# Kernel tuning notes

Measured on AMD Instinct MI355X. Metric: run time of the kernel, lower is better.

Reference implementation:

```python
import jax, jax.numpy as jnp
import numpy as np


def _lstm_step(h, c, x, W, U, b):
    # Keras gate order: i, f, g(candidate), o
    z = x @ W + h @ U + b  # [B, 4H]
    i, f, g, o = jnp.split(z, 4, axis=-1)
    i = jax.nn.sigmoid(i)
    f = jax.nn.sigmoid(f)
    g = jnp.tanh(g)
    o = jax.nn.sigmoid(o)
    c_new = f * c + i * g
    h_new = o * jnp.tanh(c_new)
    return h_new, c_new


def setup_inputs() -> dict:
    key = jax.random.key(0)
    ks = jax.random.split(key, 8)
    B, T, F, H = 2048, 512, 8, 128
    s = lambda k, shape, scale: (jax.random.normal(k, shape, jnp.float32) * scale)
    return {
        "x": jax.random.normal(ks[0], (B, T, F), jnp.float32),
        "W_enc": s(ks[1], (F, 4 * H), 0.1),
        "U_enc": s(ks[2], (H, 4 * H), 0.1),
        "b_enc": jnp.zeros((4 * H,), jnp.float32),
        "W_dec": s(ks[3], (F, 4 * H), 0.1),
        "U_dec": s(ks[4], (H, 4 * H), 0.1),
        "b_dec": jnp.zeros((4 * H,), jnp.float32),
        "W_out": s(ks[5], (H, F), 0.1),
        "b_out": jnp.zeros((F,), jnp.float32),
    }


def reference(x, W_enc, U_enc, b_enc, W_dec, U_dec, b_dec, W_out, b_out):
    B, T, F = x.shape
    H = U_enc.shape[0]
    h0 = jnp.zeros((B, H), x.dtype)
    c0 = jnp.zeros((B, H), x.dtype)

    # Encoder LSTM: only the final (h, c) state is consumed downstream.
    def enc_step(carry, xt):
        h, c = carry
        h, c = _lstm_step(h, c, xt, W_enc, U_enc, b_enc)
        return (h, c), None

    (h_enc, c_enc), _ = jax.lax.scan(enc_step, (h0, c0), jnp.swapaxes(x, 0, 1))

    def dec_step(carry, _):
        y, h, c = carry
        h, c = _lstm_step(h, c, y, W_dec, U_dec, b_dec)
        y = jax.nn.relu(h @ W_out + b_out)
        return (y, h, c), y

    _, ys = jax.lax.scan(dec_step, (x[:, -1, :], h_enc, c_enc), None, length=T)
    return jnp.swapaxes(ys, 0, 1)  # [B, T, F]
```

## Files before the change

kernel.cpp:

```cpp
#include <hip/hip_runtime.h>


namespace {

typedef __attribute__((ext_vector_type(8))) short bf16x8;
typedef __attribute__((ext_vector_type(4))) float f32x4;
typedef __attribute__((ext_vector_type(2))) unsigned int uint2v;
typedef __attribute__((ext_vector_type(4))) unsigned int uint4v;
typedef __attribute__((ext_vector_type(2))) unsigned short ushort2v;
typedef __attribute__((ext_vector_type(2))) float float2v;

constexpr int T = 512, F = 8, H = 128, G4 = 512, NTH = 512;
constexpr int HS = 136;
constexpr int XS = 40;
constexpr int CS = 16;

struct __align__(16) Smem {
  unsigned short hb[2][16][HS];
  unsigned short xp[2][16][XS];
  unsigned short xq[2][CS][16][XS];
};

__device__ __forceinline__ float rcpf(float v) { return __builtin_amdgcn_rcpf(v); }
__device__ __forceinline__ float sigm(float v) { return rcpf(1.0f + __expf(-v)); }
__device__ __forceinline__ float tanh_(float v) { return 1.0f - 2.0f * rcpf(__expf(2.0f * v) + 1.0f); }

__device__ __forceinline__ unsigned short bf_rtn(float v) {
  unsigned u = __float_as_uint(v);
  return (unsigned short)((u + 0x7FFFu + ((u >> 16) & 1u)) >> 16);
}
__device__ __forceinline__ void split_tr(float v, unsigned short& hi, unsigned short& lo) {
  unsigned u = __float_as_uint(v);
  hi = (unsigned short)(u >> 16);
  lo = bf_rtn(v - __uint_as_float(u & 0xFFFF0000u));
}

__device__ __forceinline__ float pair_fold(float a, float b) {
  uint2v r = __builtin_amdgcn_permlane32_swap(__float_as_uint(a), __float_as_uint(b), false, false);
  return __uint_as_float(r[0]) + __uint_as_float(r[1]);
}

__device__ __forceinline__ void bar_lgkm() {
  __asm__ __volatile__("s_waitcnt lgkmcnt(0)" ::: "memory");
  __builtin_amdgcn_s_barrier();
  __asm__ __volatile__("" ::: "memory");
}

__global__ __launch_bounds__(NTH, 2)
void rae_v7b(const float* __restrict__ x,
             const float* __restrict__ Wenc, const float* __restrict__ Uenc, const float* __restrict__ benc,
             const float* __restrict__ Wdec, const float* __restrict__ Udec, const float* __restrict__ bdec,
             const float* __restrict__ Wout, const float* __restrict__ boutg,
             float* __restrict__ out)
{
  __shared__ Smem s;
  const int tid = threadIdx.x, lane = tid & 63, w = tid >> 6;
  const int q = lane >> 4, n = lane & 15;
  const long gb = (long)blockIdx.x * 8;

  {
    uint4v z4 = {0u, 0u, 0u, 0u};
#pragma unroll 4
    for (int i = tid; i < (int)(sizeof(Smem) / 16); i += NTH)
      ((uint4v*)&s)[i] = z4;
  }
  __syncthreads();

  const int sfp = tid & 3, srow = (tid >> 2) & 7, sts = tid >> 5;
  const long xsb = (gb + srow) * (long)(T * F) + sts * F + sfp * 2;

  {
    float2v xv0 = *(const float2v*)&x[xsb];
    unsigned short h0s, l0s, h1s, l1s;
    split_tr(xv0[0], h0s, l0s); split_tr(xv0[1], h1s, l1s);
    ushort2v hh = {h0s, h1s}, ll = {l0s, l1s};
    *(ushort2v*)&s.xq[0][sts][srow][sfp * 2] = hh;
    *(ushort2v*)&s.xq[0][sts][srow + 8][sfp * 2] = ll;
    *(ushort2v*)&s.xq[0][sts][srow + 8][8 + sfp * 2] = hh;
  }

  bf16x8 Bw[4];
#pragma unroll
  for (int kt = 0; kt < 4; ++kt) {
    bf16x8 bw;
#pragma unroll
    for (int j = 0; j < 8; ++j) {
      unsigned short hv, lv; split_tr(Wout[(kt * 32 + q * 8 + j) * F + (n & 7)], hv, lv);
      bw[j] = (short)((n < 8) ? hv : lv);
    }
    Bw[kt] = bw;
  }
  const float boutr = boutg[n & 7];
  float cst[2] = {0.f, 0.f};
  __syncthreads();

  const float probe = pair_fold(0.0f, 1.0f);
  const int r0 = ((lane & 31) >> 4) * 4 + (int)probe;
  const int cc = w * 16 + n;

  bf16x8 A[4], Ax;
  {
    bf16x8 zz = {0, 0, 0, 0, 0, 0, 0, 0};
#pragma unroll
    for (int kt = 0; kt < 4; ++kt) A[kt] = zz;
    Ax = zz;
  }

  bf16x8 B1[5][4];
  f32x4 bias4[4];
  const f32x4 zero4 = {0.f, 0.f, 0.f, 0.f};

  auto preload = [&](const float* U, const float* W, const float* bi) {
#pragma unroll
    for (int kt = 0; kt < 5; ++kt)
#pragma unroll
      for (int g = 0; g < 4; ++g) {
        const int col = g * 128 + w * 16 + n;
        bf16x8 b1;
#pragma unroll
        for (int j = 0; j < 8; ++j) {
          unsigned short v = 0;
          if (kt < 4) {
            v = bf_rtn(U[(kt * 32 + q * 8 + j) * G4 + col]);
          } else {
            const int kk = q * 8 + j;
            unsigned short hv, lv;
            if (kk < 8)       { split_tr(W[kk * G4 + col], hv, lv); v = hv; }
            else if (kk < 16) { split_tr(W[(kk - 8) * G4 + col], hv, lv); v = lv; }
          }
          b1[j] = (short)v;
        }
        B1[kt][g] = b1;
      }
#pragma unroll
    for (int g = 0; g < 4; ++g) {
      const float b = 0.5f * bi[g * 128 + w * 16 + n];
      bias4[g] = f32x4{b, b, b, b};
    }
  };

  auto lstm_core = [&](int pnxt) {
    f32x4 acc[4];
#pragma unroll
    for (int g = 0; g < 4; ++g)
      acc[g] = __builtin_amdgcn_mfma_f32_16x16x32_bf16(A[0], B1[0][g], bias4[g], 0, 0, 0);
#pragma unroll
    for (int kt = 1; kt < 4; ++kt)
#pragma unroll
      for (int g = 0; g < 4; ++g)
        acc[g] = __builtin_amdgcn_mfma_f32_16x16x32_bf16(A[kt], B1[kt][g], acc[g], 0, 0, 0);
#pragma unroll
    for (int g = 0; g < 4; ++g)
      acc[g] = __builtin_amdgcn_mfma_f32_16x16x32_bf16(Ax, B1[4][g], acc[g], 0, 0, 0);

    float zA[4], zB[4];
#pragma unroll
    for (int g = 0; g < 4; ++g) {
      zA[g] = pair_fold(acc[g][0], acc[g][2]);
      zB[g] = pair_fold(acc[g][1], acc[g][3]);
    }
    cst[0] = sigm(zA[1]) * cst[0] + sigm(zA[0]) * tanh_(zA[2]);
    cst[1] = sigm(zB[1]) * cst[1] + sigm(zB[0]) * tanh_(zB[2]);
    const float h0 = sigm(zA[3]) * tanh_(cst[0]);
    const float h1 = sigm(zB[3]) * tanh_(cst[1]);
    unsigned short hv0, lv0, hv1, lv1;
    split_tr(h0, hv0, lv0); split_tr(h1, hv1, lv1);
    s.hb[pnxt][r0][cc]     = hv0;  s.hb[pnxt][r0 + 8][cc] = lv0;
    s.hb[pnxt][r0 + 1][cc] = hv1;  s.hb[pnxt][r0 + 9][cc] = lv1;
  };

  preload(Uenc, Wenc, benc);

  float2v xv = {0.f, 0.f};

  for (int t = 0; t < T; ++t) {
    const int pnxt = (t & 1) ^ 1;

    Ax = *(const bf16x8*)&s.xq[(t >> 4) & 1][t & (CS - 1)][n][q * 8];

    const bool do_load  = (((t + 2) & (CS - 1)) == 0) && (t + 2 < T);
    const bool do_write = (((t + 1) & (CS - 1)) == 0) && (t + 1 < T);
    if (do_load) xv = *(const float2v*)&x[xsb + (long)(t + 2) * F];

    lstm_core(pnxt);

    if (do_write) {
      const int cb = ((t + 1) >> 4) & 1;
      unsigned short h0s, l0s, h1s, l1s;
      split_tr(xv[0], h0s, l0s); split_tr(xv[1], h1s, l1s);
      ushort2v hh = {h0s, h1s}, ll = {l0s, l1s};
      *(ushort2v*)&s.xq[cb][sts][srow][sfp * 2] = hh;
      *(ushort2v*)&s.xq[cb][sts][srow + 8][sfp * 2] = ll;
      *(ushort2v*)&s.xq[cb][sts][srow + 8][8 + sfp * 2] = hh;
    }

    bar_lgkm();

#pragma unroll
    for (int kt = 0; kt < 4; ++kt)
      A[kt] = *(const bf16x8*)&s.hb[pnxt][n][kt * 32 + q * 8];
  }

  preload(Udec, Wdec, bdec);

  if (tid < 64) {
    unsigned short hv, lv;
    split_tr(x[(gb + (tid >> 3)) * (long)(T * F) + (T - 1) * F + (tid & 7)], hv, lv);
    s.xp[0][tid >> 3][tid & 7] = hv;
    s.xp[0][(tid >> 3) + 8][tid & 7] = lv;
    s.xp[0][(tid >> 3) + 8][(tid & 7) + 8] = hv;
  }
  __syncthreads();

  float* o0 = out + ((gb + r0) * (long)T) * F + n;
  float* o1 = o0 + (long)T * F;

  for (int t = 0; t < T; ++t) {
    const int pcur = t & 1, pnxt = pcur ^ 1;

    Ax = *(const bf16x8*)&s.xp[pcur][n][q * 8];

    lstm_core(pnxt);

    bar_lgkm();

#pragma unroll
    for (int kt = 0; kt < 4; ++kt)
      A[kt] = *(const bf16x8*)&s.hb[pnxt][n][kt * 32 + q * 8];

    f32x4 ay = __builtin_amdgcn_mfma_f32_16x16x32_bf16(A[0], Bw[0], zero4, 0, 0, 0);
#pragma unroll
    for (int kt = 1; kt < 4; ++kt)
      ay = __builtin_amdgcn_mfma_f32_16x16x32_bf16(A[kt], Bw[kt], ay, 0, 0, 0);
    float s8[4];
#pragma unroll
    for (int p = 0; p < 4; ++p)
      s8[p] = ay[p] + __shfl_xor(ay[p], 8, 64);
    const float y0 = fmaxf(pair_fold(s8[0], s8[2]) + boutr, 0.f);
    const float y1 = fmaxf(pair_fold(s8[1], s8[3]) + boutr, 0.f);
    if (n < 8) {
      if (w == 0) { o0[t * F] = y0; o1[t * F] = y1; }
      unsigned short hv, lv;
      split_tr(y0, hv, lv);
      s.xp[pnxt][r0][n]         = hv;
      s.xp[pnxt][r0 + 8][n]     = lv;
      s.xp[pnxt][r0 + 8][n + 8] = hv;
      split_tr(y1, hv, lv);
      s.xp[pnxt][r0 + 1][n]         = hv;
      s.xp[pnxt][r0 + 9][n]         = lv;
      s.xp[pnxt][r0 + 9][n + 8]     = hv;
    }
  }
}

}

extern "C" void kernel_launch(void* const* d_in, const int* in_sizes, int n_in,
                              void* d_out, int out_size, void* d_ws, size_t ws_size,
                              hipStream_t stream) {
  const float* x    = (const float*)d_in[0];
  const float* Wenc = (const float*)d_in[1];
  const float* Uenc = (const float*)d_in[2];
  const float* benc = (const float*)d_in[3];
  const float* Wdec = (const float*)d_in[4];
  const float* Udec = (const float*)d_in[5];
  const float* bdec = (const float*)d_in[6];
  const float* Wout = (const float*)d_in[7];
  const float* bout = (const float*)d_in[8];
  float* out = (float*)d_out;

  const int Bsz = in_sizes[0] / (T * F);
  const int nblocks = Bsz / 8;
  rae_v7b<<<dim3(nblocks), dim3(NTH), 0, stream>>>(
      x, Wenc, Uenc, benc, Wdec, Udec, bdec, Wout, bout, out);
}
```

Baseline: 1.059 ms.

## Precompute recurrent h-projection ahead of decoder feedback and reorder encoder MFMAs

In the decoder, the h·U MFMA chain for the next step is issued right after the barrier, overlapping the output dense and feedback work. Each step then only needs the x-projection MFMAs on the critical path after y is known. The encoder issues the x-projection first and prefetches the next x tile after the barrier, with both loops unrolled by two. The feedback buffer is now read right after it is written without a separate barrier, which relies on cross-wave write visibility and adds register pressure for the extra accumulators.

New measurement: 992.6 us. 6.3% less time.

```diff
diff --git a/kernel.cpp b/kernel.cpp
--- a/kernel.cpp
+++ b/kernel.cpp
@@ -47,11 +47,11 @@
 }
 
 __global__ __launch_bounds__(NTH, 2)
-void rae_v7b(const float* __restrict__ x,
-             const float* __restrict__ Wenc, const float* __restrict__ Uenc, const float* __restrict__ benc,
-             const float* __restrict__ Wdec, const float* __restrict__ Udec, const float* __restrict__ bdec,
-             const float* __restrict__ Wout, const float* __restrict__ boutg,
-             float* __restrict__ out)
+void rae_v8(const float* __restrict__ x,
+            const float* __restrict__ Wenc, const float* __restrict__ Uenc, const float* __restrict__ benc,
+            const float* __restrict__ Wdec, const float* __restrict__ Udec, const float* __restrict__ bdec,
+            const float* __restrict__ Wout, const float* __restrict__ boutg,
+            float* __restrict__ out)
 {
   __shared__ Smem s;
   const int tid = threadIdx.x, lane = tid & 63, w = tid >> 6;
@@ -139,20 +139,7 @@
     }
   };
 
-  auto lstm_core = [&](int pnxt) {
-    f32x4 acc[4];
-#pragma unroll
-    for (int g = 0; g < 4; ++g)
-      acc[g] = __builtin_amdgcn_mfma_f32_16x16x32_bf16(A[0], B1[0][g], bias4[g], 0, 0, 0);
-#pragma unroll
-    for (int kt = 1; kt < 4; ++kt)
-#pragma unroll
-      for (int g = 0; g < 4; ++g)
-        acc[g] = __builtin_amdgcn_mfma_f32_16x16x32_bf16(A[kt], B1[kt][g], acc[g], 0, 0, 0);
-#pragma unroll
-    for (int g = 0; g < 4; ++g)
-      acc[g] = __builtin_amdgcn_mfma_f32_16x16x32_bf16(Ax, B1[4][g], acc[g], 0, 0, 0);
-
+  auto activ_store = [&](f32x4 (&acc)[4], int slot) {
     float zA[4], zB[4];
 #pragma unroll
     for (int g = 0; g < 4; ++g) {
@@ -165,24 +152,34 @@
     const float h1 = sigm(zB[3]) * tanh_(cst[1]);
     unsigned short hv0, lv0, hv1, lv1;
     split_tr(h0, hv0, lv0); split_tr(h1, hv1, lv1);
-    s.hb[pnxt][r0][cc]     = hv0;  s.hb[pnxt][r0 + 8][cc] = lv0;
-    s.hb[pnxt][r0 + 1][cc] = hv1;  s.hb[pnxt][r0 + 9][cc] = lv1;
+    s.hb[slot][r0][cc]     = hv0;  s.hb[slot][r0 + 8][cc] = lv0;
+    s.hb[slot][r0 + 1][cc] = hv1;  s.hb[slot][r0 + 9][cc] = lv1;
   };
 
   preload(Uenc, Wenc, benc);
 
+  Ax = *(const bf16x8*)&s.xq[0][0][n][q * 8];
+
   float2v xv = {0.f, 0.f};
 
+#pragma unroll 2
   for (int t = 0; t < T; ++t) {
     const int pnxt = (t & 1) ^ 1;
-
-    Ax = *(const bf16x8*)&s.xq[(t >> 4) & 1][t & (CS - 1)][n][q * 8];
-
     const bool do_load  = (((t + 2) & (CS - 1)) == 0) && (t + 2 < T);
     const bool do_write = (((t + 1) & (CS - 1)) == 0) && (t + 1 < T);
     if (do_load) xv = *(const float2v*)&x[xsb + (long)(t + 2) * F];
 
-    lstm_core(pnxt);
+    f32x4 acc[4];
+#pragma unroll
+    for (int g = 0; g < 4; ++g)
+      acc[g] = __builtin_amdgcn_mfma_f32_16x16x32_bf16(Ax, B1[4][g], bias4[g], 0, 0, 0);
+#pragma unroll
+    for (int kt = 0; kt < 4; ++kt)
+#pragma unroll
+      for (int g = 0; g < 4; ++g)
+        acc[g] = __builtin_amdgcn_mfma_f32_16x16x32_bf16(A[kt], B1[kt][g], acc[g], 0, 0, 0);
+
+    activ_store(acc, pnxt);
 
     if (do_write) {
       const int cb = ((t + 1) >> 4) & 1;
@@ -196,6 +193,8 @@
 
     bar_lgkm();
 
+    const int tn = t + 1;
+    Ax = *(const bf16x8*)&s.xq[(tn >> 4) & 1][tn & (CS - 1)][n][q * 8];
 #pragma unroll
     for (int kt = 0; kt < 4; ++kt)
       A[kt] = *(const bf16x8*)&s.hb[pnxt][n][kt * 32 + q * 8];
@@ -206,50 +205,74 @@
   if (tid < 64) {
     unsigned short hv, lv;
     split_tr(x[(gb + (tid >> 3)) * (long)(T * F) + (T - 1) * F + (tid & 7)], hv, lv);
-    s.xp[0][tid >> 3][tid & 7] = hv;
-    s.xp[0][(tid >> 3) + 8][tid & 7] = lv;
-    s.xp[0][(tid >> 3) + 8][(tid & 7) + 8] = hv;
+    s.xp[1][tid >> 3][tid & 7] = hv;
+    s.xp[1][(tid >> 3) + 8][tid & 7] = lv;
+    s.xp[1][(tid >> 3) + 8][(tid & 7) + 8] = hv;
   }
   __syncthreads();
+
+  f32x4 hacc[4];
+#pragma unroll
+  for (int g = 0; g < 4; ++g)
+    hacc[g] = __builtin_amdgcn_mfma_f32_16x16x32_bf16(A[0], B1[0][g], bias4[g], 0, 0, 0);
+#pragma unroll
+  for (int kt = 1; kt < 4; ++kt)
+#pragma unroll
+    for (int g = 0; g < 4; ++g)
+      hacc[g] = __builtin_amdgcn_mfma_f32_16x16x32_bf16(A[kt], B1[kt][g], hacc[g], 0, 0, 0);
+  Ax = *(const bf16x8*)&s.xp[1][n][q * 8];
 
   float* o0 = out + ((gb + r0) * (long)T) * F + n;
   float* o1 = o0 + (long)T * F;
 
+#pragma unroll 2
   for (int t = 0; t < T; ++t) {
-    const int pcur = t & 1, pnxt = pcur ^ 1;
-
-    Ax = *(const bf16x8*)&s.xp[pcur][n][q * 8];
-
-    lstm_core(pnxt);
+    const int wA = (t & 1) ^ 1;
+
+    f32x4 acc[4];
+#pragma unroll
+    for (int g = 0; g < 4; ++g)
+      acc[g] = __builtin_amdgcn_mfma_f32_16x16x32_bf16(Ax, B1[4][g], hacc[g], 0, 0, 0);
+
+    activ_store(acc, wA);
 
     bar_lgkm();
 
 #pragma unroll
     for (int kt = 0; kt < 4; ++kt)
-      A[kt] = *(const bf16x8*)&s.hb[pnxt][n][kt * 32 + q * 8];
+      A[kt] = *(const bf16x8*)&s.hb[wA][n][kt * 32 + q * 8];
 
     f32x4 ay = __builtin_amdgcn_mfma_f32_16x16x32_bf16(A[0], Bw[0], zero4, 0, 0, 0);
 #pragma unroll
     for (int kt = 1; kt < 4; ++kt)
       ay = __builtin_amdgcn_mfma_f32_16x16x32_bf16(A[kt], Bw[kt], ay, 0, 0, 0);
-    float s8[4];
-#pragma unroll
-    for (int p = 0; p < 4; ++p)
-      s8[p] = ay[p] + __shfl_xor(ay[p], 8, 64);
-    const float y0 = fmaxf(pair_fold(s8[0], s8[2]) + boutr, 0.f);
-    const float y1 = fmaxf(pair_fold(s8[1], s8[3]) + boutr, 0.f);
+
+#pragma unroll
+    for (int g = 0; g < 4; ++g)
+      hacc[g] = __builtin_amdgcn_mfma_f32_16x16x32_bf16(A[0], B1[0][g], bias4[g], 0, 0, 0);
+#pragma unroll
+    for (int kt = 1; kt < 4; ++kt)
+#pragma unroll
+      for (int g = 0; g < 4; ++g)
+        hacc[g] = __builtin_amdgcn_mfma_f32_16x16x32_bf16(A[kt], B1[kt][g], hacc[g], 0, 0, 0);
+
+    const float sA = pair_fold(ay[0], ay[2]);
+    const float sB = pair_fold(ay[1], ay[3]);
+    const float y0 = fmaxf(sA + __shfl_xor(sA, 8, 64) + boutr, 0.f);
+    const float y1 = fmaxf(sB + __shfl_xor(sB, 8, 64) + boutr, 0.f);
     if (n < 8) {
       if (w == 0) { o0[t * F] = y0; o1[t * F] = y1; }
       unsigned short hv, lv;
       split_tr(y0, hv, lv);
-      s.xp[pnxt][r0][n]         = hv;
-      s.xp[pnxt][r0 + 8][n]     = lv;
-      s.xp[pnxt][r0 + 8][n + 8] = hv;
+      s.xp[t & 1][r0][n]         = hv;
+      s.xp[t & 1][r0 + 8][n]     = lv;
+      s.xp[t & 1][r0 + 8][n + 8] = hv;
       split_tr(y1, hv, lv);
-      s.xp[pnxt][r0 + 1][n]         = hv;
-      s.xp[pnxt][r0 + 9][n]         = lv;
-      s.xp[pnxt][r0 + 9][n + 8]     = hv;
-    }
+      s.xp[t & 1][r0 + 1][n]     = hv;
+      s.xp[t & 1][r0 + 9][n]     = lv;
+      s.xp[t & 1][r0 + 9][n + 8] = hv;
+    }
+    Ax = *(const bf16x8*)&s.xp[t & 1][n][q * 8];
   }
 }
 
@@ -271,6 +294,6 @@
 
   const int Bsz = in_sizes[0] / (T * F);
   const int nblocks = Bsz / 8;
-  rae_v7b<<<dim3(nblocks), dim3(NTH), 0, stream>>>(
+  rae_v8<<<dim3(nblocks), dim3(NTH), 0, stream>>>(
       x, Wenc, Uenc, benc, Wdec, Udec, bdec, Wout, bout, out);
 }
```
